# Optimization experiments

Measured on AMD Instinct MI355X. Metric: run time of the kernel, lower is better.

Reference implementation:

```python
import jax, jax.numpy as jnp
import numpy as np
from jax import lax

D_MODEL = 1024
D_INNER = 2048   # expand * d_model
D_STATE = 16
D_CONV = 4
DT_RANK = 64     # ceil(d_model / 16)
B_SZ, L_SEQ = 2, 2048


def setup_inputs() -> dict:
    key = jax.random.key(0)
    ks = jax.random.split(key, 12)
    s = lambda *sh: 1.0 / np.sqrt(sh[-1])
    inp = {
        "x": jax.random.normal(ks[0], (B_SZ, L_SEQ, D_MODEL), jnp.float32),
        "in_proj_w": jax.random.normal(ks[1], (2 * D_INNER, D_MODEL), jnp.float32) * s(D_MODEL),
        "conv_w": jax.random.normal(ks[2], (D_INNER, 1, D_CONV), jnp.float32) * 0.3,
        "conv_b": jax.random.normal(ks[3], (D_INNER,), jnp.float32) * 0.05,
        "x_proj_w": jax.random.normal(ks[4], (DT_RANK + 2 * D_STATE, D_INNER), jnp.float32) * s(D_INNER),
        "dt_proj_w": jax.random.normal(ks[5], (D_INNER, DT_RANK), jnp.float32) * s(DT_RANK),
        "dt_proj_b": jnp.log(jnp.exp(jax.random.uniform(ks[6], (D_INNER,), jnp.float32, 1e-3, 1e-1)) - 1.0),
        "A_log": jnp.log(jnp.broadcast_to(jnp.arange(1, D_STATE + 1, dtype=jnp.float32), (D_INNER, D_STATE))),
        "D": jnp.ones((D_INNER,), jnp.float32),
        "out_proj_w": jax.random.normal(ks[7], (D_MODEL, D_INNER), jnp.float32) * s(D_INNER),
        "ln_w": jnp.ones((D_MODEL,), jnp.float32),
        "ln_b": jnp.zeros((D_MODEL,), jnp.float32),
    }
    return inp


def _mamba(x, in_proj_w, conv_w, conv_b, x_proj_w, dt_proj_w, dt_proj_b, A_log, D, out_proj_w):
    # x: [B, L, d_model]
    xz = x @ in_proj_w.T                             # [B, L, 2*d_inner]
    u, z = jnp.split(xz, 2, axis=-1)                 # [B, L, d_inner] each
    # depthwise causal conv1d along L
    u_c = jnp.swapaxes(u, 1, 2)                      # [B, d_inner, L]
    u_c = lax.conv_general_dilated(
        u_c, conv_w, window_strides=(1,), padding=[(D_CONV - 1, 0)],
        feature_group_count=D_INNER, dimension_numbers=("NCH", "OIH", "NCH"))
    u_c = u_c + conv_b[None, :, None]
    u_c = jax.nn.silu(jnp.swapaxes(u_c, 1, 2))       # [B, L, d_inner]
    # input-dependent dt, B, C
    x_dbl = u_c @ x_proj_w.T                         # [B, L, dt_rank + 2*d_state]
    dt_lr = x_dbl[..., :DT_RANK]
    Bm = x_dbl[..., DT_RANK:DT_RANK + D_STATE]       # [B, L, d_state]
    Cm = x_dbl[..., DT_RANK + D_STATE:]              # [B, L, d_state]
    dt = jax.nn.softplus(dt_lr @ dt_proj_w.T + dt_proj_b)  # [B, L, d_inner]
    A = -jnp.exp(A_log)                              # [d_inner, d_state]

    def step(h, inputs):
        dt_t, b_t, c_t, u_t = inputs                 # [B,d_inner],[B,N],[B,N],[B,d_inner]
        dA = jnp.exp(dt_t[:, :, None] * A)           # [B, d_inner, N]
        h = h * dA + (dt_t * u_t)[:, :, None] * b_t[:, None, :]
        y_t = jnp.einsum("bdn,bn->bd", h, c_t)
        return h, y_t

    h0 = jnp.zeros((x.shape[0], D_INNER, D_STATE), x.dtype)
    xs = (jnp.swapaxes(dt, 0, 1), jnp.swapaxes(Bm, 0, 1),
          jnp.swapaxes(Cm, 0, 1), jnp.swapaxes(u_c, 0, 1))
    _, ys = lax.scan(step, h0, xs)                   # ys: [L, B, d_inner]
    y = jnp.swapaxes(ys, 0, 1) + u_c * D             # skip connection D*u
    y = y * jax.nn.silu(z)                           # gate
    return y @ out_proj_w.T                          # [B, L, d_model]


def _layernorm(x, w, b, eps=1e-5):
    mu = jnp.mean(x, axis=-1, keepdims=True)
    var = jnp.mean(jnp.square(x - mu), axis=-1, keepdims=True)
    return (x - mu) * lax.rsqrt(var + eps) * w + b


def reference(x, in_proj_w, conv_w, conv_b, x_proj_w, dt_proj_w, dt_proj_b,
              A_log, D, out_proj_w, ln_w, ln_b):
    y = _mamba(x, in_proj_w, conv_w, conv_b, x_proj_w, dt_proj_w, dt_proj_b,
               A_log, D, out_proj_w)
    return _layernorm(y + x, ln_w, ln_b)  # dropout_level=0 -> identity
```

## Files before the change

### kernel.cpp

```cpp
#include <hip/hip_runtime.h>
#include <hip/hip_bf16.h>
#include <math.h>

#define DEV static __device__ __forceinline__

typedef __hip_bfloat16 bf16;
typedef __attribute__((ext_vector_type(8))) short bf16x8;
typedef __attribute__((ext_vector_type(4))) float f32x4;

static constexpr int D_MODEL = 1024;
static constexpr int D_INNER = 2048;
static constexpr int D_STATE = 16;
static constexpr int DT_RANK = 64;
static constexpr int B_SZ   = 2;
static constexpr int L_SEQ  = 2048;
static constexpr int T_TOK  = B_SZ * L_SEQ;
static constexpr int LC     = 64;
static constexpr int NC     = L_SEQ / LC;
static constexpr int NXP    = DT_RANK + 2 * D_STATE;
static constexpr int KSPLIT = 8;

static constexpr int P_CONVW = 0;
static constexpr int P_CONVB = 8192;
static constexpr int P_DTB   = 10240;
static constexpr int P_ALOG  = 12288;
static constexpr int P_DW    = 45056;
static constexpr int P_LNW   = 47104;
static constexpr int P_LNB   = 48128;
static constexpr int P_TOT   = 49152;

DEV float bf2f(bf16 x) { return __bfloat162float(x); }
DEV bf16  f2bf(float x) { return __float2bfloat16(x); }
DEV float sigmoidf_(float x) { return 1.0f / (1.0f + __expf(-x)); }

DEV bool probe_f32(const unsigned short* probe) { return probe[1] == 0; }

DEV void async_copy16(const void* g, void* l) {
  __builtin_amdgcn_global_load_lds(
      (const __attribute__((address_space(1))) void*)g,
      (__attribute__((address_space(3))) void*)l, 16, 0, 0);
}

__global__ void cvt_all(const void* s0, const void* s1, const void* s2,
                        const void* s3, const void* s4,
                        const void* s5, const void* s6, const void* s7,
                        const void* s8, const void* s9, const void* s10,
                        const void* s11,
                        bf16* d0, bf16* d1, bf16* d2, bf16* d3, bf16* d4,
                        float* params,
                        const unsigned short* __restrict__ probe)
{
  long i = (long)(blockIdx.x * 256 + threadIdx.x) * 4;
  const void* src; long off;
  bf16* dstb = nullptr; float* dstf = nullptr;
  if      (i <  4194304) { src = s0;  dstb = d0; off = i; }
  else if (i <  8388608) { src = s1;  dstb = d1; off = i - 4194304; }
  else if (i <  8585216) { src = s2;  dstb = d2; off = i - 8388608; }
  else if (i <  8716288) { src = s3;  dstb = d3; off = i - 8585216; }
  else if (i < 10813440) { src = s4;  dstb = d4; off = i - 8716288; }
  else if (i < 10821632) { src = s5;  dstf = params + P_CONVW; off = i - 10813440; }
  else if (i < 10823680) { src = s6;  dstf = params + P_CONVB; off = i - 10821632; }
  else if (i < 10825728) { src = s7;  dstf = params + P_DTB;   off = i - 10823680; }
  else if (i < 10858496) { src = s8;  dstf = params + P_ALOG;  off = i - 10825728; }
  else if (i < 10860544) { src = s9;  dstf = params + P_DW;    off = i - 10858496; }
  else if (i < 10861568) { src = s10; dstf = params + P_LNW;   off = i - 10860544; }
  else if (i < 10862592) { src = s11; dstf = params + P_LNB;   off = i - 10861568; }
  else return;
  bool isf32 = probe_f32(probe);
  float v[4];
  if (isf32) {
    float4 t = *(const float4*)((const float*)src + off);
    v[0] = t.x; v[1] = t.y; v[2] = t.z; v[3] = t.w;
  } else {
    short4 t = *(const short4*)((const bf16*)src + off);
    v[0] = bf2f(*(bf16*)&t.x); v[1] = bf2f(*(bf16*)&t.y);
    v[2] = bf2f(*(bf16*)&t.z); v[3] = bf2f(*(bf16*)&t.w);
  }
  if (dstb) {
    #pragma unroll
    for (int k = 0; k < 4; ++k) dstb[off + k] = f2bf(v[k]);
  } else {
    #pragma unroll
    for (int k = 0; k < 4; ++k) dstf[off + k] = v[k];
  }
}

template <int MODE>
DEV void gemm_body64(const bf16* __restrict__ A, const bf16* __restrict__ B,
                     int M, int N, int K, int ld,
                     void* __restrict__ o0, void* __restrict__ o1)
{
  __shared__ __align__(16) bf16 As[128 * 64];
  __shared__ __align__(16) bf16 Bs[128 * 64];
  if (MODE == 3) {
    A += (size_t)blockIdx.z * K;
    B += (size_t)blockIdx.z * K;
  }
  const int tid  = threadIdx.x;
  const int wave = tid >> 6;
  const int lane = tid & 63;
  const int bm = blockIdx.x * 128;
  const int bn = blockIdx.y * 128;
  const int wm = (wave >> 1) * 64;
  const int wn = (wave & 1) * 64;

  f32x4 acc[4][4];
  #pragma unroll
  for (int i = 0; i < 4; ++i)
    #pragma unroll
    for (int j = 0; j < 4; ++j)
      #pragma unroll
      for (int r = 0; r < 4; ++r) acc[i][j][r] = 0.0f;

  const int srow8 = lane >> 3;
  const int sgcol = ((lane & 7) ^ srow8) * 8;
  const int fr = lane & 15;
  const int fq = lane >> 4;

  for (int k0 = 0; k0 < K; k0 += 64) {
    __syncthreads();
    #pragma unroll
    for (int rep = 0; rep < 4; ++rep) {
      int chunk = wave * 4 + rep;
      int arow = bm + chunk * 8 + srow8;
      async_copy16((const void*)(A + (size_t)arow * ld + k0 + sgcol),
                   (void*)(As + chunk * 512));
      int brow = bn + chunk * 8 + srow8;
      if (brow > N - 1) brow = N - 1;
      async_copy16((const void*)(B + (size_t)brow * ld + k0 + sgcol),
                   (void*)(Bs + chunk * 512));
    }
    __syncthreads();

    #pragma unroll
    for (int kk = 0; kk < 2; ++kk) {
      bf16x8 af[4], bg[4];
      #pragma unroll
      for (int mi = 0; mi < 4; ++mi) {
        int row = wm + mi * 16 + fr;
        af[mi] = *(const bf16x8*)(As + row * 64 + (((kk * 4 + fq) ^ (fr & 7)) * 8));
      }
      #pragma unroll
      for (int ni = 0; ni < 4; ++ni) {
        int row = wn + ni * 16 + fr;
        bg[ni] = *(const bf16x8*)(Bs + row * 64 + (((kk * 4 + fq) ^ (fr & 7)) * 8));
      }
      #pragma unroll
      for (int mi = 0; mi < 4; ++mi)
        #pragma unroll
        for (int ni = 0; ni < 4; ++ni)
          acc[mi][ni] = __builtin_amdgcn_mfma_f32_16x16x32_bf16(af[mi], bg[ni], acc[mi][ni], 0, 0, 0);
    }
  }

  const int er = (lane >> 4) * 4;
  const int ec = lane & 15;
  #pragma unroll
  for (int mi = 0; mi < 4; ++mi) {
    #pragma unroll
    for (int ni = 0; ni < 4; ++ni) {
      #pragma unroll
      for (int r = 0; r < 4; ++r) {
        int row = bm + wm + mi * 16 + er + r;
        int col = bn + wn + ni * 16 + ec;
        float v = acc[mi][ni][r];
        if (MODE == 0) {
          if (col < D_INNER) ((bf16*)o0)[(size_t)row * D_INNER + col] = f2bf(v);
          else               ((bf16*)o1)[(size_t)row * D_INNER + (col - D_INNER)] = f2bf(v * sigmoidf_(v));
        } else {
          ((float*)o0)[((size_t)blockIdx.z * M + row) * D_MODEL + col] = v;
        }
      }
    }
  }
}

template <int MODE>
DEV void gemm_body32(const bf16* __restrict__ A, const bf16* __restrict__ B,
                     int M, int N, int K, int ld,
                     void* __restrict__ o0, const void* __restrict__ e0)
{
  __shared__ __align__(16) bf16 As[128 * 32];
  __shared__ __align__(16) bf16 Bs[128 * 32];
  if (MODE == 1) {
    A += (size_t)blockIdx.z * K;
    B += (size_t)blockIdx.z * K;
  }
  const int tid  = threadIdx.x;
  const int wave = tid >> 6;
  const int lane = tid & 63;
  const int bm = blockIdx.x * 128;
  const int bn = blockIdx.y * 128;
  const int wm = (wave >> 1) * 64;
  const int wn = (wave & 1) * 64;

  f32x4 acc[4][4];
  #pragma unroll
  for (int i = 0; i < 4; ++i)
    #pragma unroll
    for (int j = 0; j < 4; ++j)
      #pragma unroll
      for (int r = 0; r < 4; ++r) acc[i][j][r] = 0.0f;

  const int ar0 = tid >> 2;
  const int ar1 = ar0 + 64;
  const int ac  = (tid & 3) * 8;
  const int fr = lane & 15;
  const int fk = (lane >> 4) * 8;

  for (int k0 = 0; k0 < K; k0 += 32) {
    bf16x8 a0 = *(const bf16x8*)(A + (size_t)(bm + ar0) * ld + k0 + ac);
    bf16x8 a1 = *(const bf16x8*)(A + (size_t)(bm + ar1) * ld + k0 + ac);
    int r0 = bn + ar0; if (r0 > N - 1) r0 = N - 1;
    int r1 = bn + ar1; if (r1 > N - 1) r1 = N - 1;
    bf16x8 b0 = *(const bf16x8*)(B + (size_t)r0 * ld + k0 + ac);
    bf16x8 b1 = *(const bf16x8*)(B + (size_t)r1 * ld + k0 + ac);
    __syncthreads();
    *(bf16x8*)(As + ar0 * 32 + ac) = a0;
    *(bf16x8*)(As + ar1 * 32 + ac) = a1;
    *(bf16x8*)(Bs + ar0 * 32 + ac) = b0;
    *(bf16x8*)(Bs + ar1 * 32 + ac) = b1;
    __syncthreads();

    bf16x8 af[4], bg[4];
    #pragma unroll
    for (int mi = 0; mi < 4; ++mi)
      af[mi] = *(const bf16x8*)(As + (wm + mi * 16 + fr) * 32 + fk);
    #pragma unroll
    for (int ni = 0; ni < 4; ++ni)
      bg[ni] = *(const bf16x8*)(Bs + (wn + ni * 16 + fr) * 32 + fk);
    #pragma unroll
    for (int mi = 0; mi < 4; ++mi)
      #pragma unroll
      for (int ni = 0; ni < 4; ++ni)
        acc[mi][ni] = __builtin_amdgcn_mfma_f32_16x16x32_bf16(af[mi], bg[ni], acc[mi][ni], 0, 0, 0);
  }

  const int er = (lane >> 4) * 4;
  const int ec = lane & 15;
  #pragma unroll
  for (int mi = 0; mi < 4; ++mi) {
    #pragma unroll
    for (int ni = 0; ni < 4; ++ni) {
      #pragma unroll
      for (int r = 0; r < 4; ++r) {
        int row = bm + wm + mi * 16 + er + r;
        int col = bn + wn + ni * 16 + ec;
        if (col >= N) continue;
        float v = acc[mi][ni][r];
        if (MODE == 1) {
          ((float*)o0)[((size_t)blockIdx.z * M + row) * N + col] = v;
        } else {
          v += ((const float*)e0)[col];
          float sp = (v > 15.0f) ? v : __logf(1.0f + __expf(v));
          ((bf16*)o0)[(size_t)row * D_INNER + col] = f2bf(sp);
        }
      }
    }
  }
}

__global__ void __launch_bounds__(256) k_inproj(const bf16* A, const bf16* B,
    void* o0, void* o1) {
  gemm_body64<0>(A, B, T_TOK, 2 * D_INNER, D_MODEL, D_MODEL, o0, o1);
}
__global__ void __launch_bounds__(256) k_outproj(const bf16* A, const bf16* B,
    void* o0) {
  gemm_body64<3>(A, B, T_TOK, D_MODEL, D_INNER / 2, D_INNER, o0, nullptr);
}
__global__ void __launch_bounds__(256) k_xproj(const bf16* A, const bf16* B,
    void* o0) {
  gemm_body32<1>(A, B, T_TOK, NXP, D_INNER / KSPLIT, D_INNER, o0, nullptr);
}
__global__ void __launch_bounds__(256) k_dtproj(const bf16* A, const bf16* B,
    void* o0, const void* e0) {
  gemm_body32<2>(A, B, T_TOK, D_INNER, DT_RANK, DT_RANK, o0, e0);
}

__global__ void xproj_post(const float* __restrict__ partials,
                           bf16* __restrict__ dtlr,
                           float* __restrict__ Bbuf,
                           float* __restrict__ Cbuf)
{
  int i = blockIdx.x * 256 + threadIdx.x;
  int col = i % NXP;
  int row = i / NXP;
  float s = 0.0f;
  #pragma unroll
  for (int kz = 0; kz < KSPLIT; ++kz)
    s += partials[((size_t)kz * T_TOK + row) * NXP + col];
  if      (col < DT_RANK)            dtlr[(size_t)row * DT_RANK + col] = f2bf(s);
  else if (col < DT_RANK + D_STATE)  Bbuf[(size_t)row * D_STATE + (col - DT_RANK)] = s;
  else                               Cbuf[(size_t)row * D_STATE + (col - DT_RANK - D_STATE)] = s;
}

__global__ void conv_silu_kernel(const bf16* __restrict__ u_pre,
                                 const float* __restrict__ cw,
                                 const float* __restrict__ cb,
                                 bf16* __restrict__ uc_bf)
{
  int idx = blockIdx.x * 256 + threadIdx.x;
  int d = idx & (D_INNER - 1);
  int t = idx >> 11;
  int l = t & (L_SEQ - 1);
  float acc = cb[d];
  #pragma unroll
  for (int w = 0; w < 4; ++w) {
    int ll = l - 3 + w;
    if (ll >= 0) acc += bf2f(u_pre[(size_t)(t - 3 + w) * D_INNER + d]) * cw[d * 4 + w];
  }
  uc_bf[idx] = f2bf(acc * sigmoidf_(acc));
}

DEV void load_Ad(const float* A_log, int d, float* Ad, bool& fast) {
  fast = true;
  #pragma unroll
  for (int n = 0; n < 16; ++n) {
    Ad[n] = -__expf(A_log[d * 16 + n]);
    fast = fast && (fabsf(Ad[n] + (float)(n + 1)) < 1e-3f * (n + 1));
  }
}
DEV void compute_decay(bool fast, float dtv, const float* Ad, float* dec) {
  if (fast) {
    float e1 = __expf(-dtv);
    float en = e1;
    #pragma unroll
    for (int n = 0; n < 16; ++n) { dec[n] = en; en *= e1; }
  } else {
    #pragma unroll
    for (int n = 0; n < 16; ++n) dec[n] = __expf(Ad[n] * dtv);
  }
}

__global__ __launch_bounds__(256) void scan_pass1(
    const bf16* __restrict__ dt, const bf16* __restrict__ uc_bf,
    const float* __restrict__ Bbuf, const float* __restrict__ A_log,
    float* __restrict__ hend, float* __restrict__ sumdt)
{
  __shared__ float Bs4[LC * D_STATE];
  __shared__ bf16 dts[16 * 256];
  __shared__ bf16 uts[16 * 256];
  int bid = blockIdx.x;
  int tid = threadIdx.x;
  int dt8 = bid & 7;
  int c = (bid >> 3) & (NC - 1);
  int b = bid >> 8;
  int d0 = dt8 * 256;
  int d  = d0 + tid;
  int t0g = b * L_SEQ + c * LC;

  ((f32x4*)Bs4)[tid] = ((const f32x4*)(Bbuf + (size_t)t0g * D_STATE))[tid];

  float Ad[16], h[16];
  bool fast;
  load_Ad(A_log, d, Ad, fast);
  #pragma unroll
  for (int n = 0; n < 16; ++n) h[n] = 0.0f;
  float sdt = 0.0f;

  for (int sub = 0; sub < 4; ++sub) {
    __syncthreads();
    #pragma unroll
    for (int rep = 0; rep < 2; ++rep) {
      int idx = rep * 256 + tid;
      int row = idx >> 5;
      int col = (idx & 31) * 8;
      size_t src = (size_t)(t0g + sub * 16 + row) * D_INNER + d0 + col;
      *(bf16x8*)(dts + row * 256 + col) = *(const bf16x8*)(dt + src);
      *(bf16x8*)(uts + row * 256 + col) = *(const bf16x8*)(uc_bf + src);
    }
    __syncthreads();
    for (int t = 0; t < 16; ++t) {
      float dtv = bf2f(dts[t * 256 + tid]);
      float uv  = bf2f(uts[t * 256 + tid]);
      float su  = dtv * uv;
      sdt += dtv;
      float dec[16];
      compute_decay(fast, dtv, Ad, dec);
      const float* Bp = Bs4 + (sub * 16 + t) * 16;
      #pragma unroll
      for (int n = 0; n < 16; ++n)
        h[n] = h[n] * dec[n] + su * Bp[n];
    }
  }
  size_t base = ((size_t)(b * NC + c) * D_INNER + d) * 16;
  #pragma unroll
  for (int q = 0; q < 4; ++q)
    *(f32x4*)(hend + base + q * 4) = *(f32x4*)(h + q * 4);
  sumdt[(size_t)(b * NC + c) * D_INNER + d] = sdt;
}

__global__ void scan_pass2(float* __restrict__ hend,
                           const float* __restrict__ sumdt,
                           const float* __restrict__ A_log)
{
  int idx = blockIdx.x * 256 + threadIdx.x;
  int n = idx & 15;
  int d = (idx >> 4) & (D_INNER - 1);
  int b = idx >> 15;
  float a = -__expf(A_log[d * 16 + n]);
  float h = 0.0f;
  for (int c = 0; c < NC; ++c) {
    size_t base = (size_t)(b * NC + c) * D_INNER + d;
    float e = hend[base * 16 + n];
    hend[base * 16 + n] = h;
    h = h * __expf(a * sumdt[base]) + e;
  }
}

__global__ __launch_bounds__(256) void scan_pass3(
    const bf16* __restrict__ dt, const bf16* __restrict__ uc_bf,
    const float* __restrict__ Bbuf, const float* __restrict__ Cbuf,
    const bf16* __restrict__ z_silu, const float* __restrict__ hstart,
    const float* __restrict__ A_log, const float* __restrict__ Dw,
    bf16* __restrict__ y_bf)
{
  __shared__ float Bs4[LC * D_STATE];
  __shared__ float Cs4[LC * D_STATE];
  __shared__ bf16 dts[16 * 256];
  __shared__ bf16 uts[16 * 256];
  __shared__ bf16 zts[16 * 256];
  int bid = blockIdx.x;
  int tid = threadIdx.x;
  int dt8 = bid & 7;
  int c = (bid >> 3) & (NC - 1);
  int b = bid >> 8;
  int d0 = dt8 * 256;
  int d  = d0 + tid;
  int t0g = b * L_SEQ + c * LC;

  ((f32x4*)Bs4)[tid] = ((const f32x4*)(Bbuf + (size_t)t0g * D_STATE))[tid];
  ((f32x4*)Cs4)[tid] = ((const f32x4*)(Cbuf + (size_t)t0g * D_STATE))[tid];

  float Ad[16], h[16];
  bool fast;
  load_Ad(A_log, d, Ad, fast);
  size_t base = ((size_t)(b * NC + c) * D_INNER + d) * 16;
  #pragma unroll
  for (int q = 0; q < 4; ++q)
    *(f32x4*)(h + q * 4) = *(const f32x4*)(hstart + base + q * 4);
  float Dv = Dw[d];

  for (int sub = 0; sub < 4; ++sub) {
    __syncthreads();
    #pragma unroll
    for (int rep = 0; rep < 2; ++rep) {
      int idx = rep * 256 + tid;
      int row = idx >> 5;
      int col = (idx & 31) * 8;
      size_t src = (size_t)(t0g + sub * 16 + row) * D_INNER + d0 + col;
      *(bf16x8*)(dts + row * 256 + col) = *(const bf16x8*)(dt + src);
      *(bf16x8*)(uts + row * 256 + col) = *(const bf16x8*)(uc_bf + src);
      *(bf16x8*)(zts + row * 256 + col) = *(const bf16x8*)(z_silu + src);
    }
    __syncthreads();
    for (int t = 0; t < 16; ++t) {
      float dtv = bf2f(dts[t * 256 + tid]);
      float uv  = bf2f(uts[t * 256 + tid]);
      float zv  = bf2f(zts[t * 256 + tid]);
      float su  = dtv * uv;
      float dec[16];
      compute_decay(fast, dtv, Ad, dec);
      const float* Bp = Bs4 + (sub * 16 + t) * 16;
      const float* Cp = Cs4 + (sub * 16 + t) * 16;
      float y = 0.0f;
      #pragma unroll
      for (int n = 0; n < 16; ++n) {
        h[n] = h[n] * dec[n] + su * Bp[n];
        y += h[n] * Cp[n];
      }
      y = (y + uv * Dv) * zv;
      y_bf[(size_t)(t0g + sub * 16 + t) * D_INNER + d] = f2bf(y);
    }
  }
}

__global__ void ln_kernel(const float* __restrict__ parts,
                          const bf16* __restrict__ x_bf,
                          const float* __restrict__ w,
                          const float* __restrict__ bia,
                          void* __restrict__ out,
                          const unsigned short* __restrict__ probe)
{
  int t = blockIdx.x;
  int tid = threadIdx.x;
  const float* p0 = parts + (size_t)t * D_MODEL;
  const float* p1 = parts + ((size_t)T_TOK + t) * D_MODEL;
  const bf16*  xr = x_bf + (size_t)t * D_MODEL;
  float v[4];
  float s = 0.0f, q = 0.0f;
  #pragma unroll
  for (int k = 0; k < 4; ++k) {
    int col = tid + k * 256;
    v[k] = p0[col] + p1[col] + bf2f(xr[col]);
    s += v[k]; q += v[k] * v[k];
  }
  #pragma unroll
  for (int off = 32; off >= 1; off >>= 1) {
    s += __shfl_down(s, off);
    q += __shfl_down(q, off);
  }
  __shared__ float red[8];
  __shared__ float mv[2];
  int wave = tid >> 6, lane = tid & 63;
  if (lane == 0) { red[wave] = s; red[4 + wave] = q; }
  __syncthreads();
  if (tid == 0) {
    float S = red[0] + red[1] + red[2] + red[3];
    float Q = red[4] + red[5] + red[6] + red[7];
    float mu = S * (1.0f / D_MODEL);
    float var = Q * (1.0f / D_MODEL) - mu * mu;
    mv[0] = mu; mv[1] = rsqrtf(var + 1e-5f);
  }
  __syncthreads();
  float mu = mv[0], rs = mv[1];
  bool isf32 = probe_f32(probe);
  #pragma unroll
  for (int k = 0; k < 4; ++k) {
    int col = tid + k * 256;
    float r = (v[k] - mu) * rs * w[col] + bia[col];
    if (isf32) ((float*)out)[(size_t)t * D_MODEL + col] = r;
    else       ((bf16*) out)[(size_t)t * D_MODEL + col] = f2bf(r);
  }
}

extern "C" void kernel_launch(void* const* d_in, const int* in_sizes, int n_in,
                              void* d_out, int out_size, void* d_ws, size_t ws_size,
                              hipStream_t stream)
{
  const void* x        = d_in[0];
  const void* in_w     = d_in[1];
  const void* conv_w   = d_in[2];
  const void* conv_b   = d_in[3];
  const void* xproj_w  = d_in[4];
  const void* dtproj_w = d_in[5];
  const void* dtproj_b = d_in[6];
  const void* A_log    = d_in[7];
  const void* Dw       = d_in[8];
  const void* out_w    = d_in[9];
  const void* ln_w     = d_in[10];
  const void* ln_b     = d_in[11];
  const unsigned short* probe = (const unsigned short*)A_log;

  char* p = (char*)d_ws;
  auto alloc = [&](size_t bytes) { char* r = p; p += (bytes + 255) & ~255ull; return r; };
  bf16*  x_bf   = (bf16*) alloc((size_t)T_TOK * D_MODEL * 2);
  bf16*  inw_bf = (bf16*) alloc((size_t)2 * D_INNER * D_MODEL * 2);
  bf16*  xpw_bf = (bf16*) alloc((size_t)NXP * D_INNER * 2);
  bf16*  dtw_bf = (bf16*) alloc((size_t)D_INNER * DT_RANK * 2);
  bf16*  outw_bf= (bf16*) alloc((size_t)D_MODEL * D_INNER * 2);
  float* params = (float*)alloc((size_t)P_TOT * 4);
  bf16*  u_pre  = (bf16*) alloc((size_t)T_TOK * D_INNER * 2);
  bf16*  z_silu = (bf16*) alloc((size_t)T_TOK * D_INNER * 2);
  bf16*  uc_bf  = (bf16*) alloc((size_t)T_TOK * D_INNER * 2);
  bf16*  dtlr   = (bf16*) alloc((size_t)T_TOK * DT_RANK * 2);
  float* Bbuf   = (float*)alloc((size_t)T_TOK * D_STATE * 4);
  float* Cbuf   = (float*)alloc((size_t)T_TOK * D_STATE * 4);
  bf16*  dtb    = (bf16*) alloc((size_t)T_TOK * D_INNER * 2);
  float* hend   = (float*)alloc((size_t)B_SZ * NC * D_INNER * 16 * 4);
  float* sumdt  = (float*)alloc((size_t)B_SZ * NC * D_INNER * 4);
  bf16*  y_bf   = u_pre;
  float* xparts = (float*)dtb;
  float* oparts = (float*)z_silu;

  dim3 blk(256);
  cvt_all<<<10608, blk, 0, stream>>>(x, in_w, xproj_w, dtproj_w, out_w,
                                     conv_w, conv_b, dtproj_b, A_log, Dw, ln_w, ln_b,
                                     x_bf, inw_bf, xpw_bf, dtw_bf, outw_bf, params, probe);

  k_inproj<<<dim3(T_TOK / 128, (2 * D_INNER) / 128), blk, 0, stream>>>(x_bf, inw_bf, u_pre, z_silu);
  conv_silu_kernel<<<(T_TOK * D_INNER) / 256, blk, 0, stream>>>(u_pre, params + P_CONVW, params + P_CONVB, uc_bf);
  k_xproj<<<dim3(T_TOK / 128, 1, KSPLIT), blk, 0, stream>>>(uc_bf, xpw_bf, xparts);
  xproj_post<<<(T_TOK * NXP) / 256, blk, 0, stream>>>(xparts, dtlr, Bbuf, Cbuf);
  k_dtproj<<<dim3(T_TOK / 128, D_INNER / 128), blk, 0, stream>>>(dtlr, dtw_bf, dtb, params + P_DTB);
  scan_pass1<<<B_SZ * NC * (D_INNER / 256), blk, 0, stream>>>(dtb, uc_bf, Bbuf, params + P_ALOG, hend, sumdt);
  scan_pass2<<<(B_SZ * D_INNER * 16) / 256, blk, 0, stream>>>(hend, sumdt, params + P_ALOG);
  scan_pass3<<<B_SZ * NC * (D_INNER / 256), blk, 0, stream>>>(
      dtb, uc_bf, Bbuf, Cbuf, z_silu, hend, params + P_ALOG, params + P_DW, y_bf);
  k_outproj<<<dim3(T_TOK / 128, D_MODEL / 128, 2), blk, 0, stream>>>(y_bf, outw_bf, oparts);
  ln_kernel<<<T_TOK, blk, 0, stream>>>(oparts, x_bf, params + P_LNW, params + P_LNB, d_out, probe);
}
```

Measured before the change: 322.5 us.

## Vectorize conv, parallelize chunk scan, and store out-proj partials in bf16

The depthwise conv+SiLU kernel now handles four channels per thread with vector loads and stores. The cross-chunk scan pass is restructured: each of four wave groups composes eight chunks, and the groups are combined through shared memory. This cuts the serial loop over 32 chunks to about 8 steps per thread. The out-projection split-K partials are written as bf16 instead of fp32, halving their traffic into the layernorm kernel at some cost in precision.

```diff
diff --git a/kernel.cpp b/kernel.cpp
--- a/kernel.cpp
+++ b/kernel.cpp
@@ -6,6 +6,7 @@
 
 typedef __hip_bfloat16 bf16;
 typedef __attribute__((ext_vector_type(8))) short bf16x8;
+typedef __attribute__((ext_vector_type(4))) short bf16x4;
 typedef __attribute__((ext_vector_type(4))) float f32x4;
 
 static constexpr int D_MODEL = 1024;
@@ -32,6 +33,8 @@
 DEV float bf2f(bf16 x) { return __bfloat162float(x); }
 DEV bf16  f2bf(float x) { return __float2bfloat16(x); }
 DEV float sigmoidf_(float x) { return 1.0f / (1.0f + __expf(-x)); }
+DEV float s2f(short s) { bf16 b; __builtin_memcpy(&b, &s, 2); return bf2f(b); }
+DEV short f2s(float x) { bf16 b = f2bf(x); short s; __builtin_memcpy(&s, &b, 2); return s; }
 
 DEV bool probe_f32(const unsigned short* probe) { return probe[1] == 0; }
 
@@ -73,8 +76,7 @@
     v[0] = t.x; v[1] = t.y; v[2] = t.z; v[3] = t.w;
   } else {
     short4 t = *(const short4*)((const bf16*)src + off);
-    v[0] = bf2f(*(bf16*)&t.x); v[1] = bf2f(*(bf16*)&t.y);
-    v[2] = bf2f(*(bf16*)&t.z); v[3] = bf2f(*(bf16*)&t.w);
+    v[0] = s2f(t.x); v[1] = s2f(t.y); v[2] = s2f(t.z); v[3] = s2f(t.w);
   }
   if (dstb) {
     #pragma unroll
@@ -168,7 +170,7 @@
           if (col < D_INNER) ((bf16*)o0)[(size_t)row * D_INNER + col] = f2bf(v);
           else               ((bf16*)o1)[(size_t)row * D_INNER + (col - D_INNER)] = f2bf(v * sigmoidf_(v));
         } else {
-          ((float*)o0)[((size_t)blockIdx.z * M + row) * D_MODEL + col] = v;
+          ((bf16*)o0)[((size_t)blockIdx.z * M + row) * D_MODEL + col] = f2bf(v);
         }
       }
     }
@@ -300,16 +302,31 @@
                                  bf16* __restrict__ uc_bf)
 {
   int idx = blockIdx.x * 256 + threadIdx.x;
-  int d = idx & (D_INNER - 1);
-  int t = idx >> 11;
-  int l = t & (L_SEQ - 1);
-  float acc = cb[d];
+  int d4 = (idx * 4) & (D_INNER - 1);
+  int t  = (idx * 4) >> 11;
+  int l  = t & (L_SEQ - 1);
+  float4 bias = *(const float4*)(cb + d4);
+  float acc[4] = {bias.x, bias.y, bias.z, bias.w};
+  float4 wv[4];
+  #pragma unroll
+  for (int i = 0; i < 4; ++i) wv[i] = *(const float4*)(cw + (d4 + i) * 4);
   #pragma unroll
   for (int w = 0; w < 4; ++w) {
-    int ll = l - 3 + w;
-    if (ll >= 0) acc += bf2f(u_pre[(size_t)(t - 3 + w) * D_INNER + d]) * cw[d * 4 + w];
-  }
-  uc_bf[idx] = f2bf(acc * sigmoidf_(acc));
+    if (l - 3 + w >= 0) {
+      bf16x4 u = *(const bf16x4*)(u_pre + (size_t)(t - 3 + w) * D_INNER + d4);
+      float uf[4];
+      #pragma unroll
+      for (int i = 0; i < 4; ++i) { short su = u[i]; uf[i] = s2f(su); }
+      acc[0] += uf[0] * ((const float*)&wv[0])[w];
+      acc[1] += uf[1] * ((const float*)&wv[1])[w];
+      acc[2] += uf[2] * ((const float*)&wv[2])[w];
+      acc[3] += uf[3] * ((const float*)&wv[3])[w];
+    }
+  }
+  bf16x4 out;
+  #pragma unroll
+  for (int i = 0; i < 4; ++i) out[i] = f2s(acc[i] * sigmoidf_(acc[i]));
+  *(bf16x4*)(uc_bf + (size_t)t * D_INNER + d4) = out;
 }
 
 DEV void load_Ad(const float* A_log, int d, float* Ad, bool& fast) {
@@ -390,21 +407,48 @@
   sumdt[(size_t)(b * NC + c) * D_INNER + d] = sdt;
 }
 
-__global__ void scan_pass2(float* __restrict__ hend,
-                           const float* __restrict__ sumdt,
-                           const float* __restrict__ A_log)
-{
-  int idx = blockIdx.x * 256 + threadIdx.x;
-  int n = idx & 15;
-  int d = (idx >> 4) & (D_INNER - 1);
-  int b = idx >> 15;
+__global__ __launch_bounds__(256) void scan_pass2(
+    float* __restrict__ hend, const float* __restrict__ sumdt,
+    const float* __restrict__ A_log)
+{
+  __shared__ float Ms[4][64];
+  __shared__ float Es[4][64];
+  int bid = blockIdx.x;
+  int tid = threadIdx.x;
+  int cg   = tid >> 6;
+  int lane = tid & 63;
+  int dloc = lane >> 4;
+  int n    = lane & 15;
+  int b     = bid >> 9;
+  int d     = (bid & 511) * 4 + dloc;
+
   float a = -__expf(A_log[d * 16 + n]);
-  float h = 0.0f;
-  for (int c = 0; c < NC; ++c) {
-    size_t base = (size_t)(b * NC + c) * D_INNER + d;
-    float e = hend[base * 16 + n];
-    hend[base * 16 + n] = h;
-    h = h * __expf(a * sumdt[base]) + e;
+
+  float Ml[8], El[8];
+  float M = 1.0f, E = 0.0f;
+  #pragma unroll
+  for (int j = 0; j < 8; ++j) {
+    int c = cg * 8 + j;
+    size_t sbase = (size_t)(b * NC + c) * D_INNER + d;
+    float m = __expf(a * sumdt[sbase]);
+    float e = hend[sbase * 16 + n];
+    Ml[j] = M; El[j] = E;
+    M = m * M;
+    E = m * E + e;
+  }
+  Ms[cg][lane] = M;
+  Es[cg][lane] = E;
+  __syncthreads();
+  float Ep = 0.0f;
+  for (int g = 0; g < cg; ++g) {
+    float Mg = Ms[g][lane], Eg = Es[g][lane];
+    Ep = Mg * Ep + Eg;
+  }
+  #pragma unroll
+  for (int j = 0; j < 8; ++j) {
+    int c = cg * 8 + j;
+    size_t sbase = (size_t)(b * NC + c) * D_INNER + d;
+    hend[sbase * 16 + n] = Ml[j] * Ep + El[j];
   }
 }
 
@@ -475,7 +519,7 @@
   }
 }
 
-__global__ void ln_kernel(const float* __restrict__ parts,
+__global__ void ln_kernel(const bf16* __restrict__ parts,
                           const bf16* __restrict__ x_bf,
                           const float* __restrict__ w,
                           const float* __restrict__ bia,
@@ -484,15 +528,15 @@
 {
   int t = blockIdx.x;
   int tid = threadIdx.x;
-  const float* p0 = parts + (size_t)t * D_MODEL;
-  const float* p1 = parts + ((size_t)T_TOK + t) * D_MODEL;
-  const bf16*  xr = x_bf + (size_t)t * D_MODEL;
+  const bf16* p0 = parts + (size_t)t * D_MODEL;
+  const bf16* p1 = parts + ((size_t)T_TOK + t) * D_MODEL;
+  const bf16* xr = x_bf + (size_t)t * D_MODEL;
   float v[4];
   float s = 0.0f, q = 0.0f;
   #pragma unroll
   for (int k = 0; k < 4; ++k) {
     int col = tid + k * 256;
-    v[k] = p0[col] + p1[col] + bf2f(xr[col]);
+    v[k] = bf2f(p0[col]) + bf2f(p1[col]) + bf2f(xr[col]);
     s += v[k]; q += v[k] * v[k];
   }
   #pragma unroll
@@ -561,7 +605,7 @@
   float* sumdt  = (float*)alloc((size_t)B_SZ * NC * D_INNER * 4);
   bf16*  y_bf   = u_pre;
   float* xparts = (float*)dtb;
-  float* oparts = (float*)z_silu;
+  bf16*  oparts = z_silu;
 
   dim3 blk(256);
   cvt_all<<<10608, blk, 0, stream>>>(x, in_w, xproj_w, dtproj_w, out_w,
@@ -569,12 +613,12 @@
                                      x_bf, inw_bf, xpw_bf, dtw_bf, outw_bf, params, probe);
 
   k_inproj<<<dim3(T_TOK / 128, (2 * D_INNER) / 128), blk, 0, stream>>>(x_bf, inw_bf, u_pre, z_silu);
-  conv_silu_kernel<<<(T_TOK * D_INNER) / 256, blk, 0, stream>>>(u_pre, params + P_CONVW, params + P_CONVB, uc_bf);
+  conv_silu_kernel<<<(T_TOK * D_INNER) / 1024, blk, 0, stream>>>(u_pre, params + P_CONVW, params + P_CONVB, uc_bf);
   k_xproj<<<dim3(T_TOK / 128, 1, KSPLIT), blk, 0, stream>>>(uc_bf, xpw_bf, xparts);
   xproj_post<<<(T_TOK * NXP) / 256, blk, 0, stream>>>(xparts, dtlr, Bbuf, Cbuf);
   k_dtproj<<<dim3(T_TOK / 128, D_INNER / 128), blk, 0, stream>>>(dtlr, dtw_bf, dtb, params + P_DTB);
   scan_pass1<<<B_SZ * NC * (D_INNER / 256), blk, 0, stream>>>(dtb, uc_bf, Bbuf, params + P_ALOG, hend, sumdt);
-  scan_pass2<<<(B_SZ * D_INNER * 16) / 256, blk, 0, stream>>>(hend, sumdt, params + P_ALOG);
+  scan_pass2<<<(B_SZ * D_INNER) / 2, blk, 0, stream>>>(hend, sumdt, params + P_ALOG);
   scan_pass3<<<B_SZ * NC * (D_INNER / 256), blk, 0, stream>>>(
       dtb, uc_bf, Bbuf, Cbuf, z_silu, hend, params + P_ALOG, params + P_DW, y_bf);
   k_outproj<<<dim3(T_TOK / 128, D_MODEL / 128, 2), blk, 0, stream>>>(y_bf, outw_bf, oparts);
```

After: 308.3 us. 4.4% less time.
